# Performance work log

Hardware: AMD Instinct MI355X
Metric: run time of the kernel (lower is better)

Reference implementation:

```python
import jax, jax.numpy as jnp
import numpy as np

EMBED_DIM = 1024
NUM_HEADS = 16
HEAD_DIM = EMBED_DIM // NUM_HEADS


def setup_inputs() -> dict:
    key = jax.random.key(0)
    k1, k2, k3, k4, k5 = jax.random.split(key, 5)
    B, N, C = 8, 1024, EMBED_DIM
    s = 1.0 / np.sqrt(C)
    return {
        "x": jax.random.normal(k1, (B, N, C), dtype=jnp.float32),
        "in_proj_weight": jax.random.normal(k2, (3 * C, C), dtype=jnp.float32) * s,
        "in_proj_bias": jax.random.normal(k3, (3 * C,), dtype=jnp.float32) * 0.02,
        "out_proj_weight": jax.random.normal(k4, (C, C), dtype=jnp.float32) * s,
        "out_proj_bias": jax.random.normal(k5, (C,), dtype=jnp.float32) * 0.02,
    }


def reference(x, in_proj_weight, in_proj_bias, out_proj_weight, out_proj_bias):
    B, N, C = x.shape
    scale = HEAD_DIM ** -0.5
    # qkv projection: F.linear(x, W, b) = x @ W.T + b -> [B, N, 3C]
    qkv = jnp.einsum("bnc,dc->bnd", x, in_proj_weight) + in_proj_bias
    # [B, N, 3, H, Dh] -> [3, B, H, N, Dh]
    qkv = qkv.reshape(B, N, 3, NUM_HEADS, HEAD_DIM).transpose(2, 0, 3, 1, 4)
    q, k, v = qkv[0], qkv[1], qkv[2]
    attn = jnp.einsum("bhqd,bhkd->bhqk", q, k) * scale
    attn = jax.nn.softmax(attn, axis=-1)
    out = jnp.einsum("bhqk,bhkd->bhqd", attn, v)
    out = out.transpose(0, 2, 1, 3).reshape(B, N, C)
    return jnp.einsum("bnc,dc->bnd", out, out_proj_weight) + out_proj_bias
```

## Files before the change

### kernel.cpp

```cpp
#include <hip/hip_runtime.h>
#include <math.h>
#include <stdint.h>

#define SEQ   1024
#define BATCH 8
#define CDIM  1024
#define HEADS 16
#define DHEAD 64

typedef __bf16 bf16;
typedef _Float16 f16;
typedef __attribute__((ext_vector_type(8))) _Float16 f16x8;
typedef __attribute__((ext_vector_type(4))) float f32x4;

static __device__ __forceinline__ void gl16(const void* g, void* l) {
    __builtin_amdgcn_global_load_lds(
        (const __attribute__((address_space(1))) void*)(uintptr_t)g,
        (__attribute__((address_space(3))) void*)(uintptr_t)l,
        16, 0, 0);
}

__global__ __launch_bounds__(256)
void cvt_all(const float* __restrict__ x,  const float* __restrict__ wi,
             const float* __restrict__ wo, f16* __restrict__ xo,
             f16* __restrict__ wio, f16* __restrict__ woo)
{
    const int N1 = 1048576, N2 = 393216;
    const int NT = N1 + N2 + 131072;
    int i = blockIdx.x * blockDim.x + threadIdx.x;
    const int stride = gridDim.x * blockDim.x;
    for (; i < NT; i += stride) {
        const float* src; f16* dst; int off;
        if (i < N1)            { src = x;  dst = xo;  off = i; }
        else if (i < N1 + N2)  { src = wi; dst = wio; off = i - N1; }
        else                   { src = wo; dst = woo; off = i - N1 - N2; }
        const f32x4 v0 = *(const f32x4*)(src + (size_t)off * 8);
        const f32x4 v1 = *(const f32x4*)(src + (size_t)off * 8 + 4);
        f16x8 o;
#pragma unroll
        for (int j = 0; j < 4; j++) {
            o[j]     = (f16)v0[j];
            o[j + 4] = (f16)v1[j];
        }
        *(f16x8*)(dst + (size_t)off * 8) = o;
    }
}

template<int MODE>
__global__ __launch_bounds__(256, 2)
void gemm_w3(const f16* __restrict__ Ag, const f16* __restrict__ Bg,
             const float* __restrict__ bias, float* __restrict__ out0,
             f16* __restrict__ qg, f16* __restrict__ kgp,
             f16* __restrict__ vgp, int Ncols, int K)
{
    __shared__ f16 As[3][4][128][8];
    __shared__ f16 Bs[3][4][256][8];

    const int m0 = blockIdx.y * 128;
    const int n0 = blockIdx.x * 256;

    const int tid  = threadIdx.x;
    const int wid  = tid >> 6;
    const int lane = tid & 63;
    const int wr   = (wid >> 1) * 64;
    const int wc   = (wid & 1) * 128;
    const int l16  = lane & 15;
    const int kgf  = lane >> 4;

    const int akg = tid >> 7, arow = tid & 127;
    const f16* aP = Ag + (size_t)(m0 + arow) * K + akg * 8;
    const f16* bP = Bg + (size_t)(n0 + tid) * K;
    const int loff = wid << 10;

#define STAGE(buf, kt)                                               \
    do {                                                             \
        gl16(aP + (kt),      (char*)As[buf] + loff);                 \
        gl16(aP + (kt) + 16, (char*)As[buf] + loff + 4096);          \
        gl16(bP + (kt),      (char*)Bs[buf] + loff);                 \
        gl16(bP + (kt) + 8,  (char*)Bs[buf] + loff + 4096);         \
        gl16(bP + (kt) + 16, (char*)Bs[buf] + loff + 8192);         \
        gl16(bP + (kt) + 24, (char*)Bs[buf] + loff + 12288);        \
    } while (0)

#define COMPUTE(buf)                                                         \
    do {                                                                     \
        f16x8 fa[4], fb[8];                                                  \
        _Pragma("unroll")                                                    \
        for (int i = 0; i < 4; i++)                                          \
            fa[i] = *(const f16x8*)&As[buf][kgf][wr + i * 16 + l16][0];      \
        _Pragma("unroll")                                                    \
        for (int j = 0; j < 8; j++)                                          \
            fb[j] = *(const f16x8*)&Bs[buf][kgf][wc + j * 16 + l16][0];      \
        __builtin_amdgcn_s_setprio(1);                                       \
        _Pragma("unroll")                                                    \
        for (int i = 0; i < 4; i++)                                          \
            _Pragma("unroll")                                                \
            for (int j = 0; j < 8; j++)                                      \
                acc[i][j] = __builtin_amdgcn_mfma_f32_16x16x32_f16(          \
                    fa[i], fb[j], acc[i][j], 0, 0, 0);                       \
        __builtin_amdgcn_s_setprio(0);                                       \
    } while (0)

    f32x4 acc[4][8];
#pragma unroll
    for (int i = 0; i < 4; i++)
#pragma unroll
        for (int j = 0; j < 8; j++) acc[i][j] = (f32x4)0.f;

    const int T = K >> 5;

    STAGE(0, 0);
    STAGE(1, 32);

    int cur = 0;
    for (int t = 0; t < T - 2; t++) {
        const int nbuf = (cur == 0) ? 2 : (cur - 1);
        STAGE(nbuf, (t + 2) << 5);
        asm volatile("s_waitcnt vmcnt(12)" ::: "memory");
        __builtin_amdgcn_sched_barrier(0);
        __builtin_amdgcn_s_barrier();
        __builtin_amdgcn_sched_barrier(0);
        COMPUTE(cur);
        __builtin_amdgcn_sched_barrier(0);
        __builtin_amdgcn_s_barrier();
        cur = (cur == 2) ? 0 : (cur + 1);
    }

    asm volatile("s_waitcnt vmcnt(6)" ::: "memory");
    __builtin_amdgcn_sched_barrier(0);
    __builtin_amdgcn_s_barrier();
    __builtin_amdgcn_sched_barrier(0);
    COMPUTE(cur);
    __builtin_amdgcn_sched_barrier(0);
    __builtin_amdgcn_s_barrier();
    cur = (cur == 2) ? 0 : (cur + 1);

    asm volatile("s_waitcnt vmcnt(0)" ::: "memory");
    __builtin_amdgcn_sched_barrier(0);
    __builtin_amdgcn_s_barrier();
    __builtin_amdgcn_sched_barrier(0);
    COMPUTE(cur);

#undef STAGE
#undef COMPUTE

#pragma unroll
    for (int j = 0; j < 8; j++) {
        const int d  = n0 + wc + j * 16 + l16;
        const float bv = bias[d];
        int s = 0, hh = 0, dh = 0;
        if (MODE == 1) {
            s  = d >> 10;
            hh = (d >> 6) & 15;
            dh = d & 63;
        }
#pragma unroll
        for (int i = 0; i < 4; i++) {
            const int mbase = m0 + wr + i * 16 + (lane >> 4) * 4;
#pragma unroll
            for (int r = 0; r < 4; r++) {
                const float v = acc[i][j][r] + bv;
                const int m = mbase + r;
                if (MODE == 0) {
                    out0[(size_t)m * Ncols + d] = v;
                } else {
                    const int b = m >> 10, n = m & 1023;
                    const size_t bho = (size_t)((b << 4) + hh) << 16;
                    if (s == 0)
                        qg[bho + ((size_t)n << 6) + dh] = (f16)(v * 0.125f);
                    else if (s == 1)
                        kgp[bho + ((size_t)n << 6) + dh] = (f16)v;
                    else
                        vgp[bho + ((size_t)dh << 10) + n] = (f16)v;
                }
            }
        }
    }
}

__global__ __launch_bounds__(256, 3)
void attn_mfma(const f16* __restrict__ qf, const f16* __restrict__ kf,
               const f16* __restrict__ vtf, f16* __restrict__ og)
{
    __shared__ f16 Kl[8][128][8];
    __shared__ f16 Vl[16][64][8];
    __shared__ f16 Pl[4][16][136];

    const int tid  = threadIdx.x;
    const int wid  = tid >> 6;
    const int lane = tid & 63;
    const int l16  = lane & 15;
    const int kg   = lane >> 4;
    const int bh   = blockIdx.y;
    const int q0   = blockIdx.x << 6;

    const size_t bhoff = (size_t)bh << 16;
    const f16* qb = qf  + bhoff;
    const f16* kb = kf  + bhoff;
    const f16* vb = vtf + bhoff;

    f16x8 qfr[2];
    {
        const f16* qrow = qb + ((size_t)(q0 + wid * 16 + l16) << 6);
        qfr[0] = *(const f16x8*)(qrow + kg * 8);
        qfr[1] = *(const f16x8*)(qrow + 32 + kg * 8);
    }

    float mrow[4], lrow[4];
    f32x4 accO[4];
#pragma unroll
    for (int r = 0; r < 4; r++) { mrow[r] = -INFINITY; lrow[r] = 0.f; }
#pragma unroll
    for (int t = 0; t < 4; t++) accO[t] = (f32x4)0.f;

    f16x8 rk[4], rv[4];
#pragma unroll
    for (int j = 0; j < 4; j++) {
        const int ck = tid + 256 * j;
        rk[j] = *(const f16x8*)(kb + ((size_t)(ck & 127) << 6) + (ck >> 7) * 8);
        rv[j] = *(const f16x8*)(vb + ((size_t)(ck & 63) << 10) + (ck >> 6) * 8);
    }

    for (int kt = 0; kt < 8; kt++) {
        __syncthreads();
#pragma unroll
        for (int j = 0; j < 4; j++) {
            const int ck = tid + 256 * j;
            *(f16x8*)&Kl[ck >> 7][ck & 127][0] = rk[j];
            *(f16x8*)&Vl[ck >> 6][ck & 63][0]  = rv[j];
        }
        __syncthreads();

        if (kt < 7) {
            const int n1 = (kt + 1) << 7;
#pragma unroll
            for (int j = 0; j < 4; j++) {
                const int ck = tid + 256 * j;
                rk[j] = *(const f16x8*)(kb + ((size_t)(n1 + (ck & 127)) << 6) + (ck >> 7) * 8);
                rv[j] = *(const f16x8*)(vb + ((size_t)(ck & 63) << 10) + n1 + (ck >> 6) * 8);
            }
        }

        f32x4 accS[8];
#pragma unroll
        for (int t = 0; t < 8; t++) accS[t] = (f32x4)0.f;
        __builtin_amdgcn_s_setprio(1);
#pragma unroll
        for (int t = 0; t < 8; t++) {
            const f16x8 kf0 = *(const f16x8*)&Kl[kg][t * 16 + l16][0];
            const f16x8 kf1 = *(const f16x8*)&Kl[4 + kg][t * 16 + l16][0];
            accS[t] = __builtin_amdgcn_mfma_f32_16x16x32_f16(qfr[0], kf0, accS[t], 0, 0, 0);
            accS[t] = __builtin_amdgcn_mfma_f32_16x16x32_f16(qfr[1], kf1, accS[t], 0, 0, 0);
        }
        __builtin_amdgcn_s_setprio(0);

#pragma unroll
        for (int r = 0; r < 4; r++) {
            float sm = fmaxf(fmaxf(fmaxf(accS[0][r], accS[1][r]),
                                   fmaxf(accS[2][r], accS[3][r])),
                             fmaxf(fmaxf(accS[4][r], accS[5][r]),
                                   fmaxf(accS[6][r], accS[7][r])));
            sm = fmaxf(sm, __shfl_xor(sm, 1, 16));
            sm = fmaxf(sm, __shfl_xor(sm, 2, 16));
            sm = fmaxf(sm, __shfl_xor(sm, 4, 16));
            sm = fmaxf(sm, __shfl_xor(sm, 8, 16));
            const float mn = fmaxf(mrow[r], sm);
            const float al = __expf(mrow[r] - mn);
            float p[8], rs = 0.f;
#pragma unroll
            for (int t = 0; t < 8; t++) {
                p[t] = __expf(accS[t][r] - mn);
                rs += p[t];
            }
            rs += __shfl_xor(rs, 1, 16);
            rs += __shfl_xor(rs, 2, 16);
            rs += __shfl_xor(rs, 4, 16);
            rs += __shfl_xor(rs, 8, 16);
            lrow[r] = lrow[r] * al + rs;
            mrow[r] = mn;
            accO[0][r] *= al;
            accO[1][r] *= al;
            accO[2][r] *= al;
            accO[3][r] *= al;
            const int prow = kg * 4 + r;
#pragma unroll
            for (int t = 0; t < 8; t++)
                Pl[wid][prow][t * 16 + l16] = (f16)p[t];
        }

        __builtin_amdgcn_s_setprio(1);
#pragma unroll
        for (int h = 0; h < 4; h++) {
            const f16x8 pa = *(const f16x8*)&Pl[wid][l16][h * 32 + kg * 8];
#pragma unroll
            for (int t = 0; t < 4; t++) {
                const f16x8 vf = *(const f16x8*)&Vl[h * 4 + kg][t * 16 + l16][0];
                accO[t] = __builtin_amdgcn_mfma_f32_16x16x32_f16(pa, vf, accO[t], 0, 0, 0);
            }
        }
        __builtin_amdgcn_s_setprio(0);
    }

    const int b = bh >> 4, hh = bh & 15;
#pragma unroll
    for (int r = 0; r < 4; r++) {
        const float inv = 1.0f / lrow[r];
        const int n = q0 + wid * 16 + kg * 4 + r;
        const size_t base = ((((size_t)b << 10) + n) << 10) + hh * 64;
#pragma unroll
        for (int t = 0; t < 4; t++)
            og[base + t * 16 + l16] = (f16)(accO[t][r] * inv);
    }
}

#define TILE 128
#define KB   16
#define LSTR (TILE + 4)

template<int MODE>
__global__ __launch_bounds__(256, 2)
void gemm_bt(const float* __restrict__ A, const float* __restrict__ Bm,
             const float* __restrict__ bias, float* __restrict__ out0,
             float* __restrict__ qg, float* __restrict__ kg, float* __restrict__ vg,
             int M, int Ncols, int K)
{
    __shared__ float As[KB][LSTR];
    __shared__ float Bs[KB][LSTR];

    const int tid = threadIdx.x;
    const int tr  = tid >> 4;
    const int tc  = tid & 15;
    const int m0  = blockIdx.y * TILE;
    const int n0  = blockIdx.x * TILE;

    const int lrow = tid >> 2;
    const int lcol = (tid & 3) << 2;

    const float* Ap = A  + (size_t)(m0 + lrow) * K + lcol;
    const float* Bp = Bm + (size_t)(n0 + lrow) * K + lcol;
    const size_t rstep = (size_t)64 * K;

    float acc[8][8];
#pragma unroll
    for (int i = 0; i < 8; i++)
#pragma unroll
        for (int j = 0; j < 8; j++) acc[i][j] = 0.f;

    for (int kt = 0; kt < K; kt += KB) {
        float4 a0 = *(const float4*)(Ap + kt);
        float4 a1 = *(const float4*)(Ap + rstep + kt);
        float4 b0 = *(const float4*)(Bp + kt);
        float4 b1 = *(const float4*)(Bp + rstep + kt);
        __syncthreads();
        As[lcol + 0][lrow]      = a0.x;
        As[lcol + 1][lrow]      = a0.y;
        As[lcol + 2][lrow]      = a0.z;
        As[lcol + 3][lrow]      = a0.w;
        As[lcol + 0][lrow + 64] = a1.x;
        As[lcol + 1][lrow + 64] = a1.y;
        As[lcol + 2][lrow + 64] = a1.z;
        As[lcol + 3][lrow + 64] = a1.w;
        Bs[lcol + 0][lrow]      = b0.x;
        Bs[lcol + 1][lrow]      = b0.y;
        Bs[lcol + 2][lrow]      = b0.z;
        Bs[lcol + 3][lrow]      = b0.w;
        Bs[lcol + 0][lrow + 64] = b1.x;
        Bs[lcol + 1][lrow + 64] = b1.y;
        Bs[lcol + 2][lrow + 64] = b1.z;
        Bs[lcol + 3][lrow + 64] = b1.w;
        __syncthreads();
#pragma unroll
        for (int kk = 0; kk < KB; kk++) {
            float ar[8], br[8];
            *(float4*)&ar[0] = *(const float4*)&As[kk][tr << 2];
            *(float4*)&ar[4] = *(const float4*)&As[kk][64 + (tr << 2)];
            *(float4*)&br[0] = *(const float4*)&Bs[kk][tc << 2];
            *(float4*)&br[4] = *(const float4*)&Bs[kk][64 + (tc << 2)];
#pragma unroll
            for (int i = 0; i < 8; i++)
#pragma unroll
                for (int j = 0; j < 8; j++)
                    acc[i][j] = fmaf(ar[i], br[j], acc[i][j]);
        }
    }

#pragma unroll
    for (int rg = 0; rg < 2; rg++) {
#pragma unroll
        for (int ri = 0; ri < 4; ri++) {
            const int m = m0 + rg * 64 + (tr << 2) + ri;
#pragma unroll
            for (int cg = 0; cg < 2; cg++) {
                const int d = n0 + cg * 64 + (tc << 2);
                const float4 bb = *(const float4*)&bias[d];
                float v0 = acc[rg * 4 + ri][cg * 4 + 0] + bb.x;
                float v1 = acc[rg * 4 + ri][cg * 4 + 1] + bb.y;
                float v2 = acc[rg * 4 + ri][cg * 4 + 2] + bb.z;
                float v3 = acc[rg * 4 + ri][cg * 4 + 3] + bb.w;
                if (MODE == 0) {
                    *(float4*)&out0[(size_t)m * Ncols + d] = make_float4(v0, v1, v2, v3);
                } else {
                    const int s  = d >> 10;
                    const int h  = (d >> 6) & 15;
                    const int dh = d & 63;
                    const int b  = m >> 10;
                    const int n  = m & 1023;
                    float* dst = (s == 0) ? qg : ((s == 1) ? kg : vg);
                    if (s == 0) { v0 *= 0.125f; v1 *= 0.125f; v2 *= 0.125f; v3 *= 0.125f; }
                    const size_t idx = (((size_t)((b << 4) + h) << 10) + n) * 64 + dh;
                    *(float4*)&dst[idx] = make_float4(v0, v1, v2, v3);
                }
            }
        }
    }
}

__global__ __launch_bounds__(256, 2)
void attn_flash_f32(const float* __restrict__ qg, const float* __restrict__ kg,
                    const float* __restrict__ vg, float* __restrict__ og)
{
    __shared__ float Qs[64][68];
    __shared__ float KPs[64][68];
    __shared__ float Vs[64][68];

    const int tid = threadIdx.x;
    const int tr  = tid >> 4;
    const int tc  = tid & 15;
    const int bh  = blockIdx.y;
    const int q0  = blockIdx.x << 6;

    const float* qb = qg + ((size_t)bh * SEQ + q0) * DHEAD;
    const float* kb = kg + (size_t)bh * SEQ * DHEAD;
    const float* vb = vg + (size_t)bh * SEQ * DHEAD;

    const int lr = tid >> 4;
    const int lc = (tid & 15) << 2;

#pragma unroll
    for (int i = 0; i < 4; i++) {
        const int r = lr + (i << 4);
        float4 t = *(const float4*)(qb + r * 64 + lc);
        Qs[lc + 0][r] = t.x;
        Qs[lc + 1][r] = t.y;
        Qs[lc + 2][r] = t.z;
        Qs[lc + 3][r] = t.w;
    }

    float m[4], l[4], acc[4][4];
#pragma unroll
    for (int i = 0; i < 4; i++) {
        m[i] = -INFINITY; l[i] = 0.f;
#pragma unroll
        for (int j = 0; j < 4; j++) acc[i][j] = 0.f;
    }

    for (int kt = 0; kt < 16; kt++) {
        __syncthreads();
        const float* kbt = kb + (size_t)(kt << 6) * 64;
        const float* vbt = vb + (size_t)(kt << 6) * 64;
#pragma unroll
        for (int i = 0; i < 4; i++) {
            const int r = lr + (i << 4);
            float4 t = *(const float4*)(kbt + r * 64 + lc);
            KPs[lc + 0][r] = t.x;
            KPs[lc + 1][r] = t.y;
            KPs[lc + 2][r] = t.z;
            KPs[lc + 3][r] = t.w;
            float4 tv = *(const float4*)(vbt + r * 64 + lc);
            *(float4*)&Vs[r][lc] = tv;
        }
        __syncthreads();

        float s[4][4];
#pragma unroll
        for (int i = 0; i < 4; i++)
#pragma unroll
            for (int j = 0; j < 4; j++) s[i][j] = 0.f;
#pragma unroll 4
        for (int d = 0; d < 64; d++) {
            float qa[4], ka[4];
            *(float4*)qa = *(const float4*)&Qs[d][tr << 2];
            *(float4*)ka = *(const float4*)&KPs[d][tc << 2];
#pragma unroll
            for (int ri = 0; ri < 4; ri++)
#pragma unroll
                for (int ci = 0; ci < 4; ci++)
                    s[ri][ci] = fmaf(qa[ri], ka[ci], s[ri][ci]);
        }
        __syncthreads();

#pragma unroll
        for (int ri = 0; ri < 4; ri++) {
            float tm = fmaxf(fmaxf(s[ri][0], s[ri][1]), fmaxf(s[ri][2], s[ri][3]));
            tm = fmaxf(tm, __shfl_xor(tm, 1, 16));
            tm = fmaxf(tm, __shfl_xor(tm, 2, 16));
            tm = fmaxf(tm, __shfl_xor(tm, 4, 16));
            tm = fmaxf(tm, __shfl_xor(tm, 8, 16));
            const float mn = fmaxf(m[ri], tm);
            const float alpha = __expf(m[ri] - mn);
            const float p0 = __expf(s[ri][0] - mn);
            const float p1 = __expf(s[ri][1] - mn);
            const float p2 = __expf(s[ri][2] - mn);
            const float p3 = __expf(s[ri][3] - mn);
            float rs = (p0 + p1) + (p2 + p3);
            rs += __shfl_xor(rs, 1, 16);
            rs += __shfl_xor(rs, 2, 16);
            rs += __shfl_xor(rs, 4, 16);
            rs += __shfl_xor(rs, 8, 16);
            l[ri] = l[ri] * alpha + rs;
            m[ri] = mn;
            acc[ri][0] *= alpha; acc[ri][1] *= alpha;
            acc[ri][2] *= alpha; acc[ri][3] *= alpha;
            *(float4*)&KPs[(tr << 2) + ri][tc << 2] = make_float4(p0, p1, p2, p3);
        }
        __syncthreads();

#pragma unroll 4
        for (int c = 0; c < 64; c += 4) {
            float pr[4][4], vv[4][4];
            *(float4*)pr[0] = *(const float4*)&KPs[(tr << 2) + 0][c];
            *(float4*)pr[1] = *(const float4*)&KPs[(tr << 2) + 1][c];
            *(float4*)pr[2] = *(const float4*)&KPs[(tr << 2) + 2][c];
            *(float4*)pr[3] = *(const float4*)&KPs[(tr << 2) + 3][c];
            *(float4*)vv[0] = *(const float4*)&Vs[c + 0][tc << 2];
            *(float4*)vv[1] = *(const float4*)&Vs[c + 1][tc << 2];
            *(float4*)vv[2] = *(const float4*)&Vs[c + 2][tc << 2];
            *(float4*)vv[3] = *(const float4*)&Vs[c + 3][tc << 2];
#pragma unroll
            for (int ri = 0; ri < 4; ri++)
#pragma unroll
                for (int j = 0; j < 4; j++) {
                    float a = acc[ri][j];
                    a = fmaf(pr[ri][0], vv[0][j], a);
                    a = fmaf(pr[ri][1], vv[1][j], a);
                    a = fmaf(pr[ri][2], vv[2][j], a);
                    a = fmaf(pr[ri][3], vv[3][j], a);
                    acc[ri][j] = a;
                }
        }
    }

    const int b = bh >> 4, h = bh & 15;
#pragma unroll
    for (int ri = 0; ri < 4; ri++) {
        const float inv = 1.0f / l[ri];
        const int n = q0 + (tr << 2) + ri;
        const size_t idx = (((size_t)b * SEQ + n) << 10) + (h << 6) + (tc << 2);
        *(float4*)&og[idx] = make_float4(acc[ri][0] * inv, acc[ri][1] * inv,
                                         acc[ri][2] * inv, acc[ri][3] * inv);
    }
}

extern "C" void kernel_launch(void* const* d_in, const int* in_sizes, int n_in,
                              void* d_out, int out_size, void* d_ws, size_t ws_size,
                              hipStream_t stream)
{
    const float* x     = (const float*)d_in[0];
    const float* w_in  = (const float*)d_in[1];
    const float* b_in  = (const float*)d_in[2];
    const float* w_out = (const float*)d_in[3];
    const float* b_out = (const float*)d_in[4];
    float* out = (float*)d_out;
    (void)in_sizes; (void)n_in; (void)out_size;

    const size_t MB  = 1024 * 1024;
    const size_t per = (size_t)BATCH * HEADS * SEQ * DHEAD;
    const int    M   = BATCH * SEQ;
    char* ws = (char*)d_ws;

    if (ws_size >= 96 * MB) {
        f16* qf16  = (f16*)(ws + 0 * MB);
        f16* kf16  = (f16*)(ws + 16 * MB);
        f16* vtf16 = (f16*)(ws + 32 * MB);
        f16* xf16  = (f16*)(ws + 48 * MB);
        f16* of16  = xf16;
        f16* wif16 = (f16*)(ws + 64 * MB);
        f16* wof16 = (f16*)(ws + 70 * MB);

        cvt_all<<<1536, 256, 0, stream>>>(x, w_in, w_out, xf16, wif16, wof16);

        gemm_w3<1><<<dim3(3 * CDIM / 256, M / 128), 256, 0, stream>>>(
            xf16, wif16, b_in, nullptr, qf16, kf16, vtf16, 3 * CDIM, CDIM);

        attn_mfma<<<dim3(SEQ / 64, BATCH * HEADS), 256, 0, stream>>>(
            qf16, kf16, vtf16, of16);

        gemm_w3<0><<<dim3(CDIM / 256, M / 128), 256, 0, stream>>>(
            of16, wof16, b_out, out, nullptr, nullptr, nullptr, CDIM, CDIM);
    } else {
        float* qws = (float*)d_ws;
        float* kws = qws + per;
        float* vws = kws + per;
        float* aws = vws + per;

        gemm_bt<1><<<dim3(3 * CDIM / TILE, M / TILE), 256, 0, stream>>>(
            x, w_in, b_in, nullptr, qws, kws, vws, M, 3 * CDIM, CDIM);

        attn_flash_f32<<<dim3(SEQ / 64, BATCH * HEADS), 256, 0, stream>>>(
            qws, kws, vws, aws);

        gemm_bt<0><<<dim3(CDIM / TILE, M / TILE), 256, 0, stream>>>(
            aws, w_out, b_out, out, nullptr, nullptr, nullptr, M, CDIM, CDIM);
    }
}
```

Baseline: 262.6 us.

## Process two 16-row query groups per wave to reuse K/V tiles in attention

Each attention block now covers 128 queries instead of 64: every wave handles two 16-row query groups that share the same K/V tiles staged in LDS. This halves the number of blocks and the total K/V global loads and LDS staging per head. In exchange each wave holds more registers (two accumulator sets, two Q fragments), so the launch bound drops from 3 to 2 blocks per CU. The grid also shrinks to 1024 blocks, which lowers parallelism.

```diff
diff --git a/kernel.cpp b/kernel.cpp
--- a/kernel.cpp
+++ b/kernel.cpp
@@ -178,7 +178,7 @@
     }
 }
 
-__global__ __launch_bounds__(256, 3)
+__global__ __launch_bounds__(256, 2)
 void attn_mfma(const f16* __restrict__ qf, const f16* __restrict__ kf,
                const f16* __restrict__ vtf, f16* __restrict__ og)
 {
@@ -192,26 +192,30 @@
     const int l16  = lane & 15;
     const int kg   = lane >> 4;
     const int bh   = blockIdx.y;
-    const int q0   = blockIdx.x << 6;
+    const int q0   = blockIdx.x << 7;
 
     const size_t bhoff = (size_t)bh << 16;
     const f16* qb = qf  + bhoff;
     const f16* kb = kf  + bhoff;
     const f16* vb = vtf + bhoff;
 
-    f16x8 qfr[2];
-    {
-        const f16* qrow = qb + ((size_t)(q0 + wid * 16 + l16) << 6);
-        qfr[0] = *(const f16x8*)(qrow + kg * 8);
-        qfr[1] = *(const f16x8*)(qrow + 32 + kg * 8);
-    }
-
-    float mrow[4], lrow[4];
-    f32x4 accO[4];
-#pragma unroll
-    for (int r = 0; r < 4; r++) { mrow[r] = -INFINITY; lrow[r] = 0.f; }
-#pragma unroll
-    for (int t = 0; t < 4; t++) accO[t] = (f32x4)0.f;
+    f16x8 qfr[2][2];
+#pragma unroll
+    for (int g = 0; g < 2; g++) {
+        const f16* qrow = qb + ((size_t)(q0 + wid * 32 + g * 16 + l16) << 6);
+        qfr[g][0] = *(const f16x8*)(qrow + kg * 8);
+        qfr[g][1] = *(const f16x8*)(qrow + 32 + kg * 8);
+    }
+
+    float mrow[2][4], lrow[2][4];
+    f32x4 accO[2][4];
+#pragma unroll
+    for (int g = 0; g < 2; g++)
+#pragma unroll
+        for (int r = 0; r < 4; r++) {
+            mrow[g][r] = -INFINITY; lrow[g][r] = 0.f;
+            accO[g][r] = (f32x4)0.f;
+        }
 
     f16x8 rk[4], rv[4];
 #pragma unroll
@@ -241,76 +245,81 @@
             }
         }
 
-        f32x4 accS[8];
-#pragma unroll
-        for (int t = 0; t < 8; t++) accS[t] = (f32x4)0.f;
-        __builtin_amdgcn_s_setprio(1);
-#pragma unroll
-        for (int t = 0; t < 8; t++) {
-            const f16x8 kf0 = *(const f16x8*)&Kl[kg][t * 16 + l16][0];
-            const f16x8 kf1 = *(const f16x8*)&Kl[4 + kg][t * 16 + l16][0];
-            accS[t] = __builtin_amdgcn_mfma_f32_16x16x32_f16(qfr[0], kf0, accS[t], 0, 0, 0);
-            accS[t] = __builtin_amdgcn_mfma_f32_16x16x32_f16(qfr[1], kf1, accS[t], 0, 0, 0);
-        }
-        __builtin_amdgcn_s_setprio(0);
-
+#pragma unroll
+        for (int g = 0; g < 2; g++) {
+            f32x4 accS[8];
+#pragma unroll
+            for (int t = 0; t < 8; t++) accS[t] = (f32x4)0.f;
+            __builtin_amdgcn_s_setprio(1);
+#pragma unroll
+            for (int t = 0; t < 8; t++) {
+                const f16x8 kf0 = *(const f16x8*)&Kl[kg][t * 16 + l16][0];
+                const f16x8 kf1 = *(const f16x8*)&Kl[4 + kg][t * 16 + l16][0];
+                accS[t] = __builtin_amdgcn_mfma_f32_16x16x32_f16(qfr[g][0], kf0, accS[t], 0, 0, 0);
+                accS[t] = __builtin_amdgcn_mfma_f32_16x16x32_f16(qfr[g][1], kf1, accS[t], 0, 0, 0);
+            }
+            __builtin_amdgcn_s_setprio(0);
+
+#pragma unroll
+            for (int r = 0; r < 4; r++) {
+                float sm = fmaxf(fmaxf(fmaxf(accS[0][r], accS[1][r]),
+                                       fmaxf(accS[2][r], accS[3][r])),
+                                 fmaxf(fmaxf(accS[4][r], accS[5][r]),
+                                       fmaxf(accS[6][r], accS[7][r])));
+                sm = fmaxf(sm, __shfl_xor(sm, 1, 16));
+                sm = fmaxf(sm, __shfl_xor(sm, 2, 16));
+                sm = fmaxf(sm, __shfl_xor(sm, 4, 16));
+                sm = fmaxf(sm, __shfl_xor(sm, 8, 16));
+                const float mn = fmaxf(mrow[g][r], sm);
+                const float al = __expf(mrow[g][r] - mn);
+                float p[8], rs = 0.f;
+#pragma unroll
+                for (int t = 0; t < 8; t++) {
+                    p[t] = __expf(accS[t][r] - mn);
+                    rs += p[t];
+                }
+                rs += __shfl_xor(rs, 1, 16);
+                rs += __shfl_xor(rs, 2, 16);
+                rs += __shfl_xor(rs, 4, 16);
+                rs += __shfl_xor(rs, 8, 16);
+                lrow[g][r] = lrow[g][r] * al + rs;
+                mrow[g][r] = mn;
+                accO[g][0][r] *= al;
+                accO[g][1][r] *= al;
+                accO[g][2][r] *= al;
+                accO[g][3][r] *= al;
+                const int prow = kg * 4 + r;
+#pragma unroll
+                for (int t = 0; t < 8; t++)
+                    Pl[wid][prow][t * 16 + l16] = (f16)p[t];
+            }
+
+            __builtin_amdgcn_s_setprio(1);
+#pragma unroll
+            for (int h = 0; h < 4; h++) {
+                const f16x8 pa = *(const f16x8*)&Pl[wid][l16][h * 32 + kg * 8];
+#pragma unroll
+                for (int t = 0; t < 4; t++) {
+                    const f16x8 vf = *(const f16x8*)&Vl[h * 4 + kg][t * 16 + l16][0];
+                    accO[g][t] = __builtin_amdgcn_mfma_f32_16x16x32_f16(pa, vf, accO[g][t], 0, 0, 0);
+                }
+            }
+            __builtin_amdgcn_s_setprio(0);
+        }
+    }
+
+    const int b = bh >> 4, hh = bh & 15;
+#pragma unroll
+    for (int g = 0; g < 2; g++)
 #pragma unroll
         for (int r = 0; r < 4; r++) {
-            float sm = fmaxf(fmaxf(fmaxf(accS[0][r], accS[1][r]),
-                                   fmaxf(accS[2][r], accS[3][r])),
-                             fmaxf(fmaxf(accS[4][r], accS[5][r]),
-                                   fmaxf(accS[6][r], accS[7][r])));
-            sm = fmaxf(sm, __shfl_xor(sm, 1, 16));
-            sm = fmaxf(sm, __shfl_xor(sm, 2, 16));
-            sm = fmaxf(sm, __shfl_xor(sm, 4, 16));
-            sm = fmaxf(sm, __shfl_xor(sm, 8, 16));
-            const float mn = fmaxf(mrow[r], sm);
-            const float al = __expf(mrow[r] - mn);
-            float p[8], rs = 0.f;
-#pragma unroll
-            for (int t = 0; t < 8; t++) {
-                p[t] = __expf(accS[t][r] - mn);
-                rs += p[t];
-            }
-            rs += __shfl_xor(rs, 1, 16);
-            rs += __shfl_xor(rs, 2, 16);
-            rs += __shfl_xor(rs, 4, 16);
-            rs += __shfl_xor(rs, 8, 16);
-            lrow[r] = lrow[r] * al + rs;
-            mrow[r] = mn;
-            accO[0][r] *= al;
-            accO[1][r] *= al;
-            accO[2][r] *= al;
-            accO[3][r] *= al;
-            const int prow = kg * 4 + r;
-#pragma unroll
-            for (int t = 0; t < 8; t++)
-                Pl[wid][prow][t * 16 + l16] = (f16)p[t];
-        }
-
-        __builtin_amdgcn_s_setprio(1);
-#pragma unroll
-        for (int h = 0; h < 4; h++) {
-            const f16x8 pa = *(const f16x8*)&Pl[wid][l16][h * 32 + kg * 8];
-#pragma unroll
-            for (int t = 0; t < 4; t++) {
-                const f16x8 vf = *(const f16x8*)&Vl[h * 4 + kg][t * 16 + l16][0];
-                accO[t] = __builtin_amdgcn_mfma_f32_16x16x32_f16(pa, vf, accO[t], 0, 0, 0);
-            }
-        }
-        __builtin_amdgcn_s_setprio(0);
-    }
-
-    const int b = bh >> 4, hh = bh & 15;
-#pragma unroll
-    for (int r = 0; r < 4; r++) {
-        const float inv = 1.0f / lrow[r];
-        const int n = q0 + wid * 16 + kg * 4 + r;
-        const size_t base = ((((size_t)b << 10) + n) << 10) + hh * 64;
-#pragma unroll
-        for (int t = 0; t < 4; t++)
-            og[base + t * 16 + l16] = (f16)(accO[t][r] * inv);
-    }
+            const float inv = 1.0f / lrow[g][r];
+            const int n = q0 + wid * 32 + g * 16 + kg * 4 + r;
+            const size_t base = ((((size_t)b << 10) + n) << 10) + hh * 64;
+#pragma unroll
+            for (int t = 0; t < 4; t++)
+                og[base + t * 16 + l16] = (f16)(accO[g][t][r] * inv);
+        }
 }
 
 #define TILE 128
@@ -582,7 +591,7 @@
         gemm_w3<1><<<dim3(3 * CDIM / 256, M / 128), 256, 0, stream>>>(
             xf16, wif16, b_in, nullptr, qf16, kf16, vtf16, 3 * CDIM, CDIM);
 
-        attn_mfma<<<dim3(SEQ / 64, BATCH * HEADS), 256, 0, stream>>>(
+        attn_mfma<<<dim3(SEQ / 128, BATCH * HEADS), 256, 0, stream>>>(
             qf16, kf16, vtf16, of16);
 
         gemm_w3<0><<<dim3(CDIM / 256, M / 128), 256, 0, stream>>>(
```

Measured after the change: 256.9 us. 1.02x faster.
